# Optimization experiments

Measured on AMD Instinct MI355X. Metric: run time of the kernel, lower is better.

Reference implementation:

```python
import jax, jax.numpy as jnp
import numpy as np

EPS = 1e-12  # F.normalize default eps: clamps norm from below


def _l2_normalize(x):
    n = jnp.sqrt(jnp.sum(x * x, axis=-1, keepdims=True))
    return x / jnp.maximum(n, EPS)


def setup_inputs() -> dict:
    key = jax.random.key(0)
    kq, kk = jax.random.split(key)
    B, N, D = 256, 65536, 3072
    query = jax.random.normal(kq, (B, D), dtype=jnp.float32)
    keys = jax.random.normal(kk, (N, D), dtype=jnp.float32)
    return {"query": query, "keys": keys, "k": 10}


def reference(query, keys, k):
    # torch.nan_to_num(query, nan=0.0, posinf=1.0, neginf=-1.0)
    q = jnp.nan_to_num(query, nan=0.0, posinf=1.0, neginf=-1.0)
    q_norm = _l2_normalize(q)            # (B, D)
    keys_norm = _l2_normalize(keys)      # (N, D) -- precomputed buffer in torch
    scores = jnp.einsum('bd,nd->bn', q_norm, keys_norm)  # cosine sims (B, N)
    _, topk_idx = jax.lax.top_k(scores, k)               # (B, k)
    top_k_embeddings = keys[topk_idx]                    # gather raw embeddings (B, k, D)
    return top_k_embeddings, topk_idx
```

## Files before the change

kernel.cpp:

```cpp
#include <hip/hip_runtime.h>
#include <math.h>

#define NQ 256
#define NK 65536
#define DD 3072
#define TOPK 10
#define BN 64
#define BK 64
#define KTILES (DD / BK)
#define ATILE_BYTES (256 * BK * 2)

typedef unsigned long long u64;
typedef unsigned int u32;
typedef unsigned short u16;

typedef __attribute__((ext_vector_type(8))) short short8;
typedef __attribute__((ext_vector_type(4))) float f32x4;
typedef __attribute__((ext_vector_type(4))) unsigned short us4;

#define GLDS(src, dst)                                                        \
  __builtin_amdgcn_global_load_lds(                                           \
      (const __attribute__((address_space(1))) void*)(src),                   \
      (__attribute__((address_space(3))) void*)(dst), 16, 0, 0)

__device__ __forceinline__ float fixv(float x) {
  if (isnan(x)) return 0.0f;
  if (isinf(x)) return x > 0.0f ? 1.0f : -1.0f;
  return x;
}

__device__ __forceinline__ u16 f2bf(float x) {
  u32 u = __float_as_uint(x);
  u32 r = (u + 0x7fffu + ((u >> 16) & 1u)) >> 16;
  return (u16)r;
}

__device__ __forceinline__ u64 makekey(float f, int idx) {
  u32 u = __float_as_uint(f);
  u = (u & 0x80000000u) ? ~u : (u | 0x80000000u);
  return ((u64)u << 32) | (u32)(~(u32)idx);
}

__global__ __launch_bounds__(256) void qnorm_kernel(const float* __restrict__ query,
                                                    float* __restrict__ qn,
                                                    u16* __restrict__ apre) {
  const int m = blockIdx.x;
  const int t = threadIdx.x;
  const float4* qp = (const float4*)(query + (size_t)m * DD);
  float4 v[3];
  float s = 0.0f;
#pragma unroll
  for (int i = 0; i < 3; ++i) {
    float4 x = qp[t + i * 256];
    x.x = fixv(x.x); x.y = fixv(x.y); x.z = fixv(x.z); x.w = fixv(x.w);
    v[i] = x;
    s += x.x * x.x + x.y * x.y + x.z * x.z + x.w * x.w;
  }
#pragma unroll
  for (int off = 32; off > 0; off >>= 1) s += __shfl_xor(s, off);
  __shared__ float red[4];
  if ((t & 63) == 0) red[t >> 6] = s;
  __syncthreads();
  float inv = 1.0f / fmaxf(sqrtf(red[0] + red[1] + red[2] + red[3]), 1e-12f);
#pragma unroll
  for (int i = 0; i < 3; ++i) {
    float4 x = v[i];
    x.x *= inv; x.y *= inv; x.z *= inv; x.w *= inv;
    ((float4*)(qn + (size_t)m * DD))[t + i * 256] = x;
    int k0 = (t + i * 256) * 4;
    int kt = k0 >> 6;
    int kk = k0 & 63;
    u32 off = (u32)kt * ATILE_BYTES + (((u32)(m * 128 + kk * 2)) ^ (((u32)m & 7) << 4));
    us4 b;
    b.x = f2bf(x.x); b.y = f2bf(x.y); b.z = f2bf(x.z); b.w = f2bf(x.w);
    *(us4*)((char*)apre + off) = b;
  }
}

__global__ __launch_bounds__(256, 3) void gemm_kernel(const u16* __restrict__ apre,
                                                      const float* __restrict__ keys,
                                                      float* __restrict__ invk,
                                                      float* __restrict__ scores) {
  __shared__ __align__(16) u16 As[256 * BK];
  __shared__ __align__(16) u16 Bs[BN * BK];
  __shared__ float sinv[BN];
  const int t = threadIdx.x;
  const int w = t >> 6, l = t & 63;
  const int n0 = blockIdx.x * BN;

  f32x4 acc[4][4];
#pragma unroll
  for (int mi = 0; mi < 4; ++mi)
#pragma unroll
    for (int ni = 0; ni < 4; ++ni) acc[mi][ni] = (f32x4){0.f, 0.f, 0.f, 0.f};
  float ssq[4] = {0.f, 0.f, 0.f, 0.f};

  const int br = t >> 4;
  const int bc = (t & 15) * 4;

  for (int kt = 0; kt < KTILES; ++kt) {
    __syncthreads();
    const char* asrc = (const char*)apre + (size_t)kt * ATILE_BYTES;
#pragma unroll
    for (int i = 0; i < 8; ++i)
      GLDS(asrc + i * 4096 + t * 16, (char*)As + i * 4096 + t * 16);
    const int kb = kt * BK;
#pragma unroll
    for (int i = 0; i < 4; ++i) {
      int row = i * 16 + br;
      float4 v = *(const float4*)(keys + (size_t)(n0 + row) * DD + kb + bc);
      ssq[i] += v.x * v.x + v.y * v.y + v.z * v.z + v.w * v.w;
      us4 b;
      b.x = f2bf(v.x); b.y = f2bf(v.y); b.z = f2bf(v.z); b.w = f2bf(v.w);
      u32 off = ((u32)(row * 128 + bc * 2)) ^ (((u32)row & 7) << 4);
      *(us4*)((char*)Bs + off) = b;
    }
    __syncthreads();
#pragma unroll
    for (int ks = 0; ks < 2; ++ks) {
      short8 a[4], b[4];
#pragma unroll
      for (int mi = 0; mi < 4; ++mi) {
        int row = w * 64 + mi * 16 + (l & 15);
        u32 off = ((u32)(row * 128 + ks * 64 + (l >> 4) * 16)) ^ (((u32)row & 7) << 4);
        a[mi] = *(const short8*)((const char*)As + off);
      }
#pragma unroll
      for (int ni = 0; ni < 4; ++ni) {
        int row = ni * 16 + (l & 15);
        u32 off = ((u32)(row * 128 + ks * 64 + (l >> 4) * 16)) ^ (((u32)row & 7) << 4);
        b[ni] = *(const short8*)((const char*)Bs + off);
      }
#pragma unroll
      for (int mi = 0; mi < 4; ++mi)
#pragma unroll
        for (int ni = 0; ni < 4; ++ni)
          acc[mi][ni] = __builtin_amdgcn_mfma_f32_16x16x32_bf16(a[mi], b[ni], acc[mi][ni], 0, 0, 0);
    }
  }

#pragma unroll
  for (int i = 0; i < 4; ++i) {
    float s = ssq[i];
    s += __shfl_xor(s, 1); s += __shfl_xor(s, 2);
    s += __shfl_xor(s, 4); s += __shfl_xor(s, 8);
    ssq[i] = s;
  }
  if ((t & 15) == 0) {
#pragma unroll
    for (int i = 0; i < 4; ++i) {
      int row = i * 16 + br;
      float iv = 1.0f / fmaxf(sqrtf(ssq[i]), 1e-12f);
      sinv[row] = iv;
      invk[n0 + row] = iv;
    }
  }
  __syncthreads();

#pragma unroll
  for (int ni = 0; ni < 4; ++ni) {
    int nl = ni * 16 + (l & 15);
    float iv = sinv[nl];
#pragma unroll
    for (int mi = 0; mi < 4; ++mi) {
      int q = w * 64 + mi * 16 + (l >> 4) * 4;
#pragma unroll
      for (int r = 0; r < 4; ++r)
        scores[(size_t)(q + r) * NK + n0 + nl] = acc[mi][ni][r] * iv;
    }
  }
}

__global__ __launch_bounds__(256) void topk_part(const float* __restrict__ scores,
                                                 u64* __restrict__ cand) {
  const int b = blockIdx.x >> 3, p = blockIdx.x & 7;
  const int t = threadIdx.x;
  const int w = t >> 6, l = t & 63;
  const float4* row4 = (const float4*)(scores + (size_t)b * NK) + p * 2048;

  float4 v[8];
#pragma unroll
  for (int i = 0; i < 8; ++i) v[i] = row4[i * 256 + t];

  u64 c16[16];
#pragma unroll
  for (int i = 0; i < 4; ++i) {
    int nb = (p * 2048 + i * 256 + t) * 4;
    c16[i * 4 + 0] = makekey(v[i].x, nb + 0);
    c16[i * 4 + 1] = makekey(v[i].y, nb + 1);
    c16[i * 4 + 2] = makekey(v[i].z, nb + 2);
    c16[i * 4 + 3] = makekey(v[i].w, nb + 3);
  }
  u64 mn = c16[0];
#pragma unroll
  for (int i = 1; i < 16; ++i) mn = c16[i] < mn ? c16[i] : mn;

#pragma unroll
  for (int i = 4; i < 8; ++i) {
    int nb = (p * 2048 + i * 256 + t) * 4;
    float e[4] = {v[i].x, v[i].y, v[i].z, v[i].w};
#pragma unroll
    for (int j = 0; j < 4; ++j) {
      u64 kk = makekey(e[j], nb + j);
      if (kk > mn) {
#pragma unroll
        for (int q = 0; q < 16; ++q)
          if (c16[q] == mn) c16[q] = kk;
        u64 m2 = c16[0];
#pragma unroll
        for (int q = 1; q < 16; ++q) m2 = c16[q] < m2 ? c16[q] : m2;
        mn = m2;
      }
    }
  }

#pragma unroll 1
  for (int r = 0; r < 16; ++r) {
    u64 best = 0;
#pragma unroll
    for (int i = 0; i < 16; ++i) best = c16[i] > best ? c16[i] : best;
    u64 wb = best;
#pragma unroll
    for (int off = 1; off < 64; off <<= 1) {
      u64 o = __shfl_xor(wb, off);
      wb = o > wb ? o : wb;
    }
#pragma unroll
    for (int i = 0; i < 16; ++i)
      if (c16[i] == wb) c16[i] = 0;
    if (l == 0) cand[(((size_t)b * 8 + p) * 4 + w) * 16 + r] = wb;
  }
}

__global__ __launch_bounds__(256) void merge_rescore(const u64* __restrict__ cand,
                                                     const float* __restrict__ qn,
                                                     const float* __restrict__ keys,
                                                     const float* __restrict__ invk,
                                                     float* __restrict__ out_emb,
                                                     float* __restrict__ out_idx) {
  const int b = blockIdx.x;
  const int t = threadIdx.x;
  const int w = t >> 6, l = t & 63;
  __shared__ u64 top16[16];
  __shared__ float exact[16];
  __shared__ int ord[TOPK];

  if (w == 0) {
    u64 lc[8];
    const u64* cb = cand + (size_t)b * 512;
#pragma unroll
    for (int i = 0; i < 8; ++i) lc[i] = cb[l * 8 + i];
#pragma unroll 1
    for (int r = 0; r < 16; ++r) {
      u64 best = 0;
#pragma unroll
      for (int i = 0; i < 8; ++i) best = lc[i] > best ? lc[i] : best;
      u64 wb = best;
#pragma unroll
      for (int off = 1; off < 64; off <<= 1) {
        u64 o = __shfl_xor(wb, off);
        wb = o > wb ? o : wb;
      }
#pragma unroll
      for (int i = 0; i < 8; ++i)
        if (lc[i] == wb) lc[i] = 0;
      if (l == 0) top16[r] = wb;
    }
  }
  __syncthreads();

  {
    const int g = t >> 4, c = t & 15;
    const int idx = (int)(~(u32)top16[g]);
    const float iv = invk[idx];
    const float4* kp = (const float4*)(keys + (size_t)idx * DD);
    const float4* qp = (const float4*)(qn + (size_t)b * DD);
    float s = 0.0f;
    for (int j = 0; j < 48; ++j) {
      float4 kv = kp[j * 16 + c];
      float4 qv = qp[j * 16 + c];
      s = fmaf(qv.x, kv.x * iv, s);
      s = fmaf(qv.y, kv.y * iv, s);
      s = fmaf(qv.z, kv.z * iv, s);
      s = fmaf(qv.w, kv.w * iv, s);
    }
    s += __shfl_xor(s, 1); s += __shfl_xor(s, 2);
    s += __shfl_xor(s, 4); s += __shfl_xor(s, 8);
    if (c == 0) exact[g] = s;
  }
  __syncthreads();

  if (w == 0 && l < 16) {
    u64 ek = makekey(exact[l], (int)(~(u32)top16[l]));
#pragma unroll 1
    for (int r = 0; r < TOPK; ++r) {
      u64 wb = ek;
#pragma unroll
      for (int off = 1; off < 16; off <<= 1) {
        u64 o = __shfl_xor(wb, off);
        wb = o > wb ? o : wb;
      }
      if (wb == ek) ek = 0;
      if (l == 0) ord[r] = (int)(~(u32)wb);
    }
  }
  __syncthreads();

  for (int r = 0; r < TOPK; ++r) {
    int idx = ord[r];
    if (t == 0) out_idx[b * TOPK + r] = (float)idx;
    const float4* src = (const float4*)(keys + (size_t)idx * DD);
    float4* dst = (float4*)(out_emb + ((size_t)b * TOPK + r) * DD);
#pragma unroll
    for (int c2 = 0; c2 < 3; ++c2) dst[t + c2 * 256] = src[t + c2 * 256];
  }
}

extern "C" void kernel_launch(void* const* d_in, const int* in_sizes, int n_in,
                              void* d_out, int out_size, void* d_ws, size_t ws_size,
                              hipStream_t stream) {
  const float* query = (const float*)d_in[0];
  const float* keys  = (const float*)d_in[1];

  float* ws = (float*)d_ws;
  float* invk   = ws;
  float* qn     = ws + NK;
  u16*   apre   = (u16*)(ws + NK + (size_t)NQ * DD);
  float* scores = ws + NK + (size_t)NQ * DD + (size_t)KTILES * 256 * BK / 2;
  u64*   cand   = (u64*)(scores + (size_t)NQ * NK);

  float* out_emb = (float*)d_out;
  float* out_idx = (float*)d_out + (size_t)NQ * TOPK * DD;

  qnorm_kernel<<<NQ, 256, 0, stream>>>(query, qn, apre);
  gemm_kernel<<<NK / BN, 256, 0, stream>>>(apre, keys, invk, scores);
  topk_part<<<NQ * 8, 256, 0, stream>>>(scores, cand);
  merge_rescore<<<NQ, 256, 0, stream>>>(cand, qn, keys, invk, out_emb, out_idx);
}
```

Baseline: 323.9 us.

## Fuse per-tile top-k selection into GEMM epilogue and prefetch key tiles

```diff
diff --git a/kernel.cpp b/kernel.cpp
--- a/kernel.cpp
+++ b/kernel.cpp
@@ -9,6 +9,7 @@
 #define BK 64
 #define KTILES (DD / BK)
 #define ATILE_BYTES (256 * BK * 2)
+#define CPB 8
 
 typedef unsigned long long u64;
 typedef unsigned int u32;
@@ -39,6 +40,12 @@
   u32 u = __float_as_uint(f);
   u = (u & 0x80000000u) ? ~u : (u | 0x80000000u);
   return ((u64)u << 32) | (u32)(~(u32)idx);
+}
+
+__device__ __forceinline__ u64 skey(u16 bf, int idx) {
+  u32 s = ((u32)bf) << 16;
+  s = (s & 0x80000000u) ? ~s : (s | 0x80000000u);
+  return ((u64)s << 32) | (u32)(~(u32)idx);
 }
 
 __global__ __launch_bounds__(256) void qnorm_kernel(const float* __restrict__ query,
@@ -77,10 +84,10 @@
   }
 }
 
-__global__ __launch_bounds__(256, 3) void gemm_kernel(const u16* __restrict__ apre,
-                                                      const float* __restrict__ keys,
-                                                      float* __restrict__ invk,
-                                                      float* __restrict__ scores) {
+__global__ __launch_bounds__(256, 3) void gemm_topk(const u16* __restrict__ apre,
+                                                    const float* __restrict__ keys,
+                                                    float* __restrict__ invk,
+                                                    u64* __restrict__ cand) {
   __shared__ __align__(16) u16 As[256 * BK];
   __shared__ __align__(16) u16 Bs[BN * BK];
   __shared__ float sinv[BN];
@@ -98,24 +105,34 @@
   const int br = t >> 4;
   const int bc = (t & 15) * 4;
 
+  float4 bpf[4];
+#pragma unroll
+  for (int i = 0; i < 4; ++i)
+    bpf[i] = *(const float4*)(keys + (size_t)(n0 + i * 16 + br) * DD + bc);
+
   for (int kt = 0; kt < KTILES; ++kt) {
     __syncthreads();
     const char* asrc = (const char*)apre + (size_t)kt * ATILE_BYTES;
 #pragma unroll
     for (int i = 0; i < 8; ++i)
       GLDS(asrc + i * 4096 + t * 16, (char*)As + i * 4096 + t * 16);
-    const int kb = kt * BK;
 #pragma unroll
     for (int i = 0; i < 4; ++i) {
-      int row = i * 16 + br;
-      float4 v = *(const float4*)(keys + (size_t)(n0 + row) * DD + kb + bc);
+      float4 v = bpf[i];
       ssq[i] += v.x * v.x + v.y * v.y + v.z * v.z + v.w * v.w;
       us4 b;
       b.x = f2bf(v.x); b.y = f2bf(v.y); b.z = f2bf(v.z); b.w = f2bf(v.w);
+      int row = i * 16 + br;
       u32 off = ((u32)(row * 128 + bc * 2)) ^ (((u32)row & 7) << 4);
       *(us4*)((char*)Bs + off) = b;
     }
     __syncthreads();
+    if (kt < KTILES - 1) {
+      const int kb = (kt + 1) * BK;
+#pragma unroll
+      for (int i = 0; i < 4; ++i)
+        bpf[i] = *(const float4*)(keys + (size_t)(n0 + i * 16 + br) * DD + kb + bc);
+    }
 #pragma unroll
     for (int ks = 0; ks < 2; ++ks) {
       short8 a[4], b[4];
@@ -163,73 +180,47 @@
     float iv = sinv[nl];
 #pragma unroll
     for (int mi = 0; mi < 4; ++mi) {
-      int q = w * 64 + mi * 16 + (l >> 4) * 4;
-#pragma unroll
-      for (int r = 0; r < 4; ++r)
-        scores[(size_t)(q + r) * NK + n0 + nl] = acc[mi][ni][r] * iv;
-    }
-  }
-}
-
-__global__ __launch_bounds__(256) void topk_part(const float* __restrict__ scores,
-                                                 u64* __restrict__ cand) {
-  const int b = blockIdx.x >> 3, p = blockIdx.x & 7;
-  const int t = threadIdx.x;
-  const int w = t >> 6, l = t & 63;
-  const float4* row4 = (const float4*)(scores + (size_t)b * NK) + p * 2048;
-
-  float4 v[8];
-#pragma unroll
-  for (int i = 0; i < 8; ++i) v[i] = row4[i * 256 + t];
-
-  u64 c16[16];
-#pragma unroll
-  for (int i = 0; i < 4; ++i) {
-    int nb = (p * 2048 + i * 256 + t) * 4;
-    c16[i * 4 + 0] = makekey(v[i].x, nb + 0);
-    c16[i * 4 + 1] = makekey(v[i].y, nb + 1);
-    c16[i * 4 + 2] = makekey(v[i].z, nb + 2);
-    c16[i * 4 + 3] = makekey(v[i].w, nb + 3);
-  }
-  u64 mn = c16[0];
-#pragma unroll
-  for (int i = 1; i < 16; ++i) mn = c16[i] < mn ? c16[i] : mn;
-
-#pragma unroll
-  for (int i = 4; i < 8; ++i) {
-    int nb = (p * 2048 + i * 256 + t) * 4;
-    float e[4] = {v[i].x, v[i].y, v[i].z, v[i].w};
-#pragma unroll
-    for (int j = 0; j < 4; ++j) {
-      u64 kk = makekey(e[j], nb + j);
+      int qb = w * 64 + mi * 16 + (l >> 4) * 4;
+#pragma unroll
+      for (int r = 0; r < 4; ++r) {
+        int q = qb + r;
+        u16 bf = f2bf(acc[mi][ni][r] * iv);
+        u32 off = ((u32)(q * 128 + nl * 2)) ^ (((u32)q & 7) << 4);
+        *(u16*)((char*)As + off) = bf;
+      }
+    }
+  }
+  __syncthreads();
+
+  u64 c8[CPB];
+  {
+    short8 v = *(const short8*)((const char*)As + (((u32)(t * 128)) ^ (((u32)t & 7) << 4)));
+#pragma unroll
+    for (int j = 0; j < 8; ++j) c8[j] = skey((u16)v[j], n0 + j);
+  }
+  u64 mn = c8[0];
+#pragma unroll
+  for (int i = 1; i < CPB; ++i) mn = c8[i] < mn ? c8[i] : mn;
+#pragma unroll
+  for (int c = 1; c < 8; ++c) {
+    short8 v = *(const short8*)((const char*)As + (((u32)(t * 128 + c * 16)) ^ (((u32)t & 7) << 4)));
+#pragma unroll
+    for (int j = 0; j < 8; ++j) {
+      u64 kk = skey((u16)v[j], n0 + c * 8 + j);
       if (kk > mn) {
 #pragma unroll
-        for (int q = 0; q < 16; ++q)
-          if (c16[q] == mn) c16[q] = kk;
-        u64 m2 = c16[0];
-#pragma unroll
-        for (int q = 1; q < 16; ++q) m2 = c16[q] < m2 ? c16[q] : m2;
+        for (int q = 0; q < CPB; ++q)
+          if (c8[q] == mn) c8[q] = kk;
+        u64 m2 = c8[0];
+#pragma unroll
+        for (int q = 1; q < CPB; ++q) m2 = c8[q] < m2 ? c8[q] : m2;
         mn = m2;
       }
     }
   }
-
-#pragma unroll 1
-  for (int r = 0; r < 16; ++r) {
-    u64 best = 0;
-#pragma unroll
-    for (int i = 0; i < 16; ++i) best = c16[i] > best ? c16[i] : best;
-    u64 wb = best;
-#pragma unroll
-    for (int off = 1; off < 64; off <<= 1) {
-      u64 o = __shfl_xor(wb, off);
-      wb = o > wb ? o : wb;
-    }
-#pragma unroll
-    for (int i = 0; i < 16; ++i)
-      if (c16[i] == wb) c16[i] = 0;
-    if (l == 0) cand[(((size_t)b * 8 + p) * 4 + w) * 16 + r] = wb;
-  }
+  u64* cp = cand + ((size_t)t * (NK / BN) + blockIdx.x) * CPB;
+#pragma unroll
+  for (int i = 0; i < CPB; ++i) cp[i] = c8[i];
 }
 
 __global__ __launch_bounds__(256) void merge_rescore(const u64* __restrict__ cand,
@@ -241,29 +232,59 @@
   const int b = blockIdx.x;
   const int t = threadIdx.x;
   const int w = t >> 6, l = t & 63;
+  __shared__ u64 wtop[64];
   __shared__ u64 top16[16];
   __shared__ float exact[16];
   __shared__ int ord[TOPK];
 
+  const u64* cb = cand + (size_t)b * (NK / BN) * CPB;
+  u64 c16[16];
+#pragma unroll
+  for (int i = 0; i < 16; ++i) c16[i] = cb[t * 32 + i];
+  u64 mn = c16[0];
+#pragma unroll
+  for (int i = 1; i < 16; ++i) mn = c16[i] < mn ? c16[i] : mn;
+#pragma unroll
+  for (int i = 16; i < 32; ++i) {
+    u64 kk = cb[t * 32 + i];
+    if (kk > mn) {
+#pragma unroll
+      for (int q = 0; q < 16; ++q)
+        if (c16[q] == mn) c16[q] = kk;
+      u64 m2 = c16[0];
+#pragma unroll
+      for (int q = 1; q < 16; ++q) m2 = c16[q] < m2 ? c16[q] : m2;
+      mn = m2;
+    }
+  }
+#pragma unroll 1
+  for (int r = 0; r < 16; ++r) {
+    u64 best = 0;
+#pragma unroll
+    for (int i = 0; i < 16; ++i) best = c16[i] > best ? c16[i] : best;
+    u64 wb = best;
+#pragma unroll
+    for (int off = 1; off < 64; off <<= 1) {
+      u64 o = __shfl_xor(wb, off);
+      wb = o > wb ? o : wb;
+    }
+#pragma unroll
+    for (int i = 0; i < 16; ++i)
+      if (c16[i] == wb) c16[i] = 0;
+    if (l == 0) wtop[w * 16 + r] = wb;
+  }
+  __syncthreads();
   if (w == 0) {
-    u64 lc[8];
-    const u64* cb = cand + (size_t)b * 512;
-#pragma unroll
-    for (int i = 0; i < 8; ++i) lc[i] = cb[l * 8 + i];
+    u64 e = wtop[l];
 #pragma unroll 1
     for (int r = 0; r < 16; ++r) {
-      u64 best = 0;
-#pragma unroll
-      for (int i = 0; i < 8; ++i) best = lc[i] > best ? lc[i] : best;
-      u64 wb = best;
+      u64 wb = e;
 #pragma unroll
       for (int off = 1; off < 64; off <<= 1) {
         u64 o = __shfl_xor(wb, off);
         wb = o > wb ? o : wb;
       }
-#pragma unroll
-      for (int i = 0; i < 8; ++i)
-        if (lc[i] == wb) lc[i] = 0;
+      if (e == wb) e = 0;
       if (l == 0) top16[r] = wb;
     }
   }
@@ -323,17 +344,15 @@
   const float* keys  = (const float*)d_in[1];
 
   float* ws = (float*)d_ws;
-  float* invk   = ws;
-  float* qn     = ws + NK;
-  u16*   apre   = (u16*)(ws + NK + (size_t)NQ * DD);
-  float* scores = ws + NK + (size_t)NQ * DD + (size_t)KTILES * 256 * BK / 2;
-  u64*   cand   = (u64*)(scores + (size_t)NQ * NK);
+  float* invk = ws;
+  float* qn   = ws + NK;
+  u16*   apre = (u16*)(ws + NK + (size_t)NQ * DD);
+  u64*   cand = (u64*)((char*)(void*)apre + (size_t)KTILES * ATILE_BYTES);
 
   float* out_emb = (float*)d_out;
   float* out_idx = (float*)d_out + (size_t)NQ * TOPK * DD;
 
   qnorm_kernel<<<NQ, 256, 0, stream>>>(query, qn, apre);
-  gemm_kernel<<<NK / BN, 256, 0, stream>>>(apre, keys, invk, scores);
-  topk_part<<<NQ * 8, 256, 0, stream>>>(scores, cand);
+  gemm_topk<<<NK / BN, 256, 0, stream>>>(apre, keys, invk, cand);
   merge_rescore<<<NQ, 256, 0, stream>>>(cand, qn, keys, invk, out_emb, out_idx);
 }
```

Result: slower. 332.6 us (+2.7%).

## Double-buffer fp32 key tiles via direct LDS loads and read A fragments from global

Applied to the files above, without the earlier changes.

```diff
diff --git a/kernel.cpp b/kernel.cpp
--- a/kernel.cpp
+++ b/kernel.cpp
@@ -8,7 +8,6 @@
 #define BN 64
 #define BK 64
 #define KTILES (DD / BK)
-#define ATILE_BYTES (256 * BK * 2)
 
 typedef unsigned long long u64;
 typedef unsigned int u32;
@@ -17,6 +16,7 @@
 typedef __attribute__((ext_vector_type(8))) short short8;
 typedef __attribute__((ext_vector_type(4))) float f32x4;
 typedef __attribute__((ext_vector_type(4))) unsigned short us4;
+typedef __attribute__((ext_vector_type(4))) unsigned int u32x4;
 
 #define GLDS(src, dst)                                                        \
   __builtin_amdgcn_global_load_lds(                                           \
@@ -70,10 +70,9 @@
     int k0 = (t + i * 256) * 4;
     int kt = k0 >> 6;
     int kk = k0 & 63;
-    u32 off = (u32)kt * ATILE_BYTES + (((u32)(m * 128 + kk * 2)) ^ (((u32)m & 7) << 4));
     us4 b;
     b.x = f2bf(x.x); b.y = f2bf(x.y); b.z = f2bf(x.z); b.w = f2bf(x.w);
-    *(us4*)((char*)apre + off) = b;
+    *(us4*)(apre + ((size_t)kt * 256 + m) * 64 + kk) = b;
   }
 }
 
@@ -81,8 +80,7 @@
                                                       const float* __restrict__ keys,
                                                       float* __restrict__ invk,
                                                       float* __restrict__ scores) {
-  __shared__ __align__(16) u16 As[256 * BK];
-  __shared__ __align__(16) u16 Bs[BN * BK];
+  __shared__ __align__(16) float Bf[2][BN * BK];
   __shared__ float sinv[BN];
   const int t = threadIdx.x;
   const int w = t >> 6, l = t & 63;
@@ -93,64 +91,86 @@
   for (int mi = 0; mi < 4; ++mi)
 #pragma unroll
     for (int ni = 0; ni < 4; ++ni) acc[mi][ni] = (f32x4){0.f, 0.f, 0.f, 0.f};
-  float ssq[4] = {0.f, 0.f, 0.f, 0.f};
-
-  const int br = t >> 4;
-  const int bc = (t & 15) * 4;
+  float ssq_acc = 0.0f;
+
+#define STAGE_B(kt_, buf_)                                                    \
+  {                                                                           \
+    const int kb_ = (kt_)*BK;                                                 \
+    _Pragma("unroll")                                                         \
+    for (int i_ = 0; i_ < 4; ++i_) {                                          \
+      int c_ = w * 256 + i_ * 64 + l;                                         \
+      int row_ = c_ >> 4;                                                     \
+      int kc_ = (c_ & 15) ^ (row_ & 7);                                       \
+      GLDS(keys + (size_t)(n0 + row_) * DD + kb_ + kc_ * 4,                   \
+           (char*)&Bf[buf_][0] + c_ * 16);                                    \
+    }                                                                         \
+  }
+
+  STAGE_B(0, 0);
 
   for (int kt = 0; kt < KTILES; ++kt) {
     __syncthreads();
-    const char* asrc = (const char*)apre + (size_t)kt * ATILE_BYTES;
-#pragma unroll
-    for (int i = 0; i < 8; ++i)
-      GLDS(asrc + i * 4096 + t * 16, (char*)As + i * 4096 + t * 16);
-    const int kb = kt * BK;
-#pragma unroll
-    for (int i = 0; i < 4; ++i) {
-      int row = i * 16 + br;
-      float4 v = *(const float4*)(keys + (size_t)(n0 + row) * DD + kb + bc);
-      ssq[i] += v.x * v.x + v.y * v.y + v.z * v.z + v.w * v.w;
-      us4 b;
-      b.x = f2bf(v.x); b.y = f2bf(v.y); b.z = f2bf(v.z); b.w = f2bf(v.w);
-      u32 off = ((u32)(row * 128 + bc * 2)) ^ (((u32)row & 7) << 4);
-      *(us4*)((char*)Bs + off) = b;
-    }
-    __syncthreads();
+    const int cur = kt & 1;
+
+    short8 af[8];
+    {
+      const u16* ab = apre + (size_t)kt * 256 * 64;
+#pragma unroll
+      for (int mi = 0; mi < 4; ++mi)
+#pragma unroll
+        for (int ks = 0; ks < 2; ++ks)
+          af[mi * 2 + ks] = *(const short8*)(ab +
+              (size_t)(w * 64 + mi * 16 + (l & 15)) * 64 + ks * 32 + (l >> 4) * 8);
+    }
+    __builtin_amdgcn_sched_barrier(0);
+    if (kt + 1 < KTILES) STAGE_B(kt + 1, cur ^ 1);
+    __builtin_amdgcn_sched_barrier(0);
+
+    {
+      const int row = t >> 2;
+#pragma unroll
+      for (int j = 0; j < 4; ++j) {
+        int kc = (t & 3) * 4 + j;
+        f32x4 v = *(const f32x4*)((const char*)&Bf[cur][0] +
+                                  (row * 16 + (kc ^ (row & 7))) * 16);
+        ssq_acc += v.x * v.x + v.y * v.y + v.z * v.z + v.w * v.w;
+      }
+    }
+
 #pragma unroll
     for (int ks = 0; ks < 2; ++ks) {
-      short8 a[4], b[4];
-#pragma unroll
-      for (int mi = 0; mi < 4; ++mi) {
-        int row = w * 64 + mi * 16 + (l & 15);
-        u32 off = ((u32)(row * 128 + ks * 64 + (l >> 4) * 16)) ^ (((u32)row & 7) << 4);
-        a[mi] = *(const short8*)((const char*)As + off);
-      }
+      short8 b[4];
 #pragma unroll
       for (int ni = 0; ni < 4; ++ni) {
         int row = ni * 16 + (l & 15);
-        u32 off = ((u32)(row * 128 + ks * 64 + (l >> 4) * 16)) ^ (((u32)row & 7) << 4);
-        b[ni] = *(const short8*)((const char*)Bs + off);
+        int kc0 = ks * 8 + (l >> 4) * 2;
+        u32x4 p0 = *(const u32x4*)((const char*)&Bf[cur][0] +
+                                   (row * 16 + (kc0 ^ (row & 7))) * 16);
+        u32x4 p1 = *(const u32x4*)((const char*)&Bf[cur][0] +
+                                   (row * 16 + ((kc0 + 1) ^ (row & 7))) * 16);
+        u32x4 bw;
+        bw.x = (p0.x >> 16) | (p0.y & 0xffff0000u);
+        bw.y = (p0.z >> 16) | (p0.w & 0xffff0000u);
+        bw.z = (p1.x >> 16) | (p1.y & 0xffff0000u);
+        bw.w = (p1.z >> 16) | (p1.w & 0xffff0000u);
+        b[ni] = *(short8*)&bw;
       }
 #pragma unroll
       for (int mi = 0; mi < 4; ++mi)
 #pragma unroll
         for (int ni = 0; ni < 4; ++ni)
-          acc[mi][ni] = __builtin_amdgcn_mfma_f32_16x16x32_bf16(a[mi], b[ni], acc[mi][ni], 0, 0, 0);
-    }
-  }
-
-#pragma unroll
-  for (int i = 0; i < 4; ++i) {
-    float s = ssq[i];
-    s += __shfl_xor(s, 1); s += __shfl_xor(s, 2);
-    s += __shfl_xor(s, 4); s += __shfl_xor(s, 8);
-    ssq[i] = s;
-  }
-  if ((t & 15) == 0) {
-#pragma unroll
-    for (int i = 0; i < 4; ++i) {
-      int row = i * 16 + br;
-      float iv = 1.0f / fmaxf(sqrtf(ssq[i]), 1e-12f);
+          acc[mi][ni] = __builtin_amdgcn_mfma_f32_16x16x32_bf16(
+              af[mi * 2 + ks], b[ni], acc[mi][ni], 0, 0, 0);
+    }
+  }
+
+  {
+    float s = ssq_acc;
+    s += __shfl_xor(s, 1);
+    s += __shfl_xor(s, 2);
+    if ((t & 3) == 0) {
+      int row = t >> 2;
+      float iv = 1.0f / fmaxf(sqrtf(s), 1e-12f);
       sinv[row] = iv;
       invk[n0 + row] = iv;
     }
```

Result: slower. 390.7 us (+20.6%).

## Widen GEMM blocks to 512 threads, fuse top-k with merge, split gather

Applied to the files above, without the earlier changes.

```diff
diff --git a/kernel.cpp b/kernel.cpp
--- a/kernel.cpp
+++ b/kernel.cpp
@@ -77,7 +77,7 @@
   }
 }
 
-__global__ __launch_bounds__(256, 3) void gemm_kernel(const u16* __restrict__ apre,
+__global__ __launch_bounds__(512, 4) void gemm_kernel(const u16* __restrict__ apre,
                                                       const float* __restrict__ keys,
                                                       float* __restrict__ invk,
                                                       float* __restrict__ scores) {
@@ -88,40 +88,43 @@
   const int w = t >> 6, l = t & 63;
   const int n0 = blockIdx.x * BN;
 
-  f32x4 acc[4][4];
-#pragma unroll
-  for (int mi = 0; mi < 4; ++mi)
+  f32x4 acc[2][4];
+#pragma unroll
+  for (int mi = 0; mi < 2; ++mi)
 #pragma unroll
     for (int ni = 0; ni < 4; ++ni) acc[mi][ni] = (f32x4){0.f, 0.f, 0.f, 0.f};
-  float ssq[4] = {0.f, 0.f, 0.f, 0.f};
-
-  const int br = t >> 4;
-  const int bc = (t & 15) * 4;
+  float ssq = 0.0f;
+
+  const int brow = t >> 3;
+  const int bco = (t & 7) * 8;
 
   for (int kt = 0; kt < KTILES; ++kt) {
     __syncthreads();
     const char* asrc = (const char*)apre + (size_t)kt * ATILE_BYTES;
 #pragma unroll
-    for (int i = 0; i < 8; ++i)
-      GLDS(asrc + i * 4096 + t * 16, (char*)As + i * 4096 + t * 16);
+    for (int i = 0; i < 4; ++i)
+      GLDS(asrc + i * 8192 + t * 16, (char*)As + i * 8192 + t * 16);
     const int kb = kt * BK;
-#pragma unroll
-    for (int i = 0; i < 4; ++i) {
-      int row = i * 16 + br;
-      float4 v = *(const float4*)(keys + (size_t)(n0 + row) * DD + kb + bc);
-      ssq[i] += v.x * v.x + v.y * v.y + v.z * v.z + v.w * v.w;
-      us4 b;
-      b.x = f2bf(v.x); b.y = f2bf(v.y); b.z = f2bf(v.z); b.w = f2bf(v.w);
-      u32 off = ((u32)(row * 128 + bc * 2)) ^ (((u32)row & 7) << 4);
-      *(us4*)((char*)Bs + off) = b;
+    {
+      const float* bp = keys + (size_t)(n0 + brow) * DD + kb + bco;
+      float4 v0 = *(const float4*)(bp);
+      float4 v1 = *(const float4*)(bp + 4);
+      ssq += v0.x * v0.x + v0.y * v0.y + v0.z * v0.z + v0.w * v0.w +
+             v1.x * v1.x + v1.y * v1.y + v1.z * v1.z + v1.w * v1.w;
+      us4 b0, b1;
+      b0.x = f2bf(v0.x); b0.y = f2bf(v0.y); b0.z = f2bf(v0.z); b0.w = f2bf(v0.w);
+      b1.x = f2bf(v1.x); b1.y = f2bf(v1.y); b1.z = f2bf(v1.z); b1.w = f2bf(v1.w);
+      u32 off = ((u32)(brow * 128 + bco * 2)) ^ (((u32)brow & 7) << 4);
+      *(us4*)((char*)Bs + off) = b0;
+      *(us4*)((char*)Bs + off + 8) = b1;
     }
     __syncthreads();
 #pragma unroll
     for (int ks = 0; ks < 2; ++ks) {
-      short8 a[4], b[4];
-#pragma unroll
-      for (int mi = 0; mi < 4; ++mi) {
-        int row = w * 64 + mi * 16 + (l & 15);
+      short8 a[2], b[4];
+#pragma unroll
+      for (int mi = 0; mi < 2; ++mi) {
+        int row = w * 32 + mi * 16 + (l & 15);
         u32 off = ((u32)(row * 128 + ks * 64 + (l >> 4) * 16)) ^ (((u32)row & 7) << 4);
         a[mi] = *(const short8*)((const char*)As + off);
       }
@@ -132,27 +135,20 @@
         b[ni] = *(const short8*)((const char*)Bs + off);
       }
 #pragma unroll
-      for (int mi = 0; mi < 4; ++mi)
+      for (int mi = 0; mi < 2; ++mi)
 #pragma unroll
         for (int ni = 0; ni < 4; ++ni)
           acc[mi][ni] = __builtin_amdgcn_mfma_f32_16x16x32_bf16(a[mi], b[ni], acc[mi][ni], 0, 0, 0);
     }
   }
 
-#pragma unroll
-  for (int i = 0; i < 4; ++i) {
-    float s = ssq[i];
-    s += __shfl_xor(s, 1); s += __shfl_xor(s, 2);
-    s += __shfl_xor(s, 4); s += __shfl_xor(s, 8);
-    ssq[i] = s;
-  }
-  if ((t & 15) == 0) {
-#pragma unroll
-    for (int i = 0; i < 4; ++i) {
-      int row = i * 16 + br;
-      float iv = 1.0f / fmaxf(sqrtf(ssq[i]), 1e-12f);
-      sinv[row] = iv;
-      invk[n0 + row] = iv;
+  {
+    float s = ssq;
+    s += __shfl_xor(s, 1); s += __shfl_xor(s, 2); s += __shfl_xor(s, 4);
+    if ((t & 7) == 0) {
+      float iv = 1.0f / fmaxf(sqrtf(s), 1e-12f);
+      sinv[brow] = iv;
+      invk[n0 + brow] = iv;
     }
   }
   __syncthreads();
@@ -162,8 +158,8 @@
     int nl = ni * 16 + (l & 15);
     float iv = sinv[nl];
 #pragma unroll
-    for (int mi = 0; mi < 4; ++mi) {
-      int q = w * 64 + mi * 16 + (l >> 4) * 4;
+    for (int mi = 0; mi < 2; ++mi) {
+      int q = w * 32 + mi * 16 + (l >> 4) * 4;
 #pragma unroll
       for (int r = 0; r < 4; ++r)
         scores[(size_t)(q + r) * NK + n0 + nl] = acc[mi][ni][r] * iv;
@@ -171,34 +167,39 @@
   }
 }
 
-__global__ __launch_bounds__(256) void topk_part(const float* __restrict__ scores,
-                                                 u64* __restrict__ cand) {
-  const int b = blockIdx.x >> 3, p = blockIdx.x & 7;
+__global__ __launch_bounds__(256) void topk_merge(const float* __restrict__ scores,
+                                                  const float* __restrict__ qn,
+                                                  const float* __restrict__ keys,
+                                                  const float* __restrict__ invk,
+                                                  int* __restrict__ ordws,
+                                                  float* __restrict__ out_idx) {
+  const int b = blockIdx.x;
   const int t = threadIdx.x;
   const int w = t >> 6, l = t & 63;
-  const float4* row4 = (const float4*)(scores + (size_t)b * NK) + p * 2048;
-
-  float4 v[8];
-#pragma unroll
-  for (int i = 0; i < 8; ++i) v[i] = row4[i * 256 + t];
+  const float4* row4 = (const float4*)(scores + (size_t)b * NK);
+  __shared__ u64 wtop[64];
+  __shared__ u64 top16[16];
+  __shared__ float exact[16];
 
   u64 c16[16];
 #pragma unroll
   for (int i = 0; i < 4; ++i) {
-    int nb = (p * 2048 + i * 256 + t) * 4;
-    c16[i * 4 + 0] = makekey(v[i].x, nb + 0);
-    c16[i * 4 + 1] = makekey(v[i].y, nb + 1);
-    c16[i * 4 + 2] = makekey(v[i].z, nb + 2);
-    c16[i * 4 + 3] = makekey(v[i].w, nb + 3);
+    float4 v = row4[i * 256 + t];
+    int nb = (i * 256 + t) * 4;
+    c16[i * 4 + 0] = makekey(v.x, nb + 0);
+    c16[i * 4 + 1] = makekey(v.y, nb + 1);
+    c16[i * 4 + 2] = makekey(v.z, nb + 2);
+    c16[i * 4 + 3] = makekey(v.w, nb + 3);
   }
   u64 mn = c16[0];
 #pragma unroll
   for (int i = 1; i < 16; ++i) mn = c16[i] < mn ? c16[i] : mn;
 
-#pragma unroll
-  for (int i = 4; i < 8; ++i) {
-    int nb = (p * 2048 + i * 256 + t) * 4;
-    float e[4] = {v[i].x, v[i].y, v[i].z, v[i].w};
+#pragma unroll 4
+  for (int i = 4; i < 64; ++i) {
+    float4 v = row4[i * 256 + t];
+    int nb = (i * 256 + t) * 4;
+    float e[4] = {v.x, v.y, v.z, v.w};
 #pragma unroll
     for (int j = 0; j < 4; ++j) {
       u64 kk = makekey(e[j], nb + j);
@@ -228,42 +229,20 @@
 #pragma unroll
     for (int i = 0; i < 16; ++i)
       if (c16[i] == wb) c16[i] = 0;
-    if (l == 0) cand[(((size_t)b * 8 + p) * 4 + w) * 16 + r] = wb;
-  }
-}
-
-__global__ __launch_bounds__(256) void merge_rescore(const u64* __restrict__ cand,
-                                                     const float* __restrict__ qn,
-                                                     const float* __restrict__ keys,
-                                                     const float* __restrict__ invk,
-                                                     float* __restrict__ out_emb,
-                                                     float* __restrict__ out_idx) {
-  const int b = blockIdx.x;
-  const int t = threadIdx.x;
-  const int w = t >> 6, l = t & 63;
-  __shared__ u64 top16[16];
-  __shared__ float exact[16];
-  __shared__ int ord[TOPK];
-
+    if (l == 0) wtop[w * 16 + r] = wb;
+  }
+  __syncthreads();
   if (w == 0) {
-    u64 lc[8];
-    const u64* cb = cand + (size_t)b * 512;
-#pragma unroll
-    for (int i = 0; i < 8; ++i) lc[i] = cb[l * 8 + i];
+    u64 e = wtop[l];
 #pragma unroll 1
     for (int r = 0; r < 16; ++r) {
-      u64 best = 0;
-#pragma unroll
-      for (int i = 0; i < 8; ++i) best = lc[i] > best ? lc[i] : best;
-      u64 wb = best;
+      u64 wb = e;
 #pragma unroll
       for (int off = 1; off < 64; off <<= 1) {
         u64 o = __shfl_xor(wb, off);
         wb = o > wb ? o : wb;
       }
-#pragma unroll
-      for (int i = 0; i < 8; ++i)
-        if (lc[i] == wb) lc[i] = 0;
+      if (e == wb) e = 0;
       if (l == 0) top16[r] = wb;
     }
   }
@@ -301,19 +280,24 @@
         wb = o > wb ? o : wb;
       }
       if (wb == ek) ek = 0;
-      if (l == 0) ord[r] = (int)(~(u32)wb);
-    }
-  }
-  __syncthreads();
-
-  for (int r = 0; r < TOPK; ++r) {
-    int idx = ord[r];
-    if (t == 0) out_idx[b * TOPK + r] = (float)idx;
-    const float4* src = (const float4*)(keys + (size_t)idx * DD);
-    float4* dst = (float4*)(out_emb + ((size_t)b * TOPK + r) * DD);
-#pragma unroll
-    for (int c2 = 0; c2 < 3; ++c2) dst[t + c2 * 256] = src[t + c2 * 256];
-  }
+      if (l == 0) {
+        int idx = (int)(~(u32)wb);
+        ordws[b * TOPK + r] = idx;
+        out_idx[b * TOPK + r] = (float)idx;
+      }
+    }
+  }
+}
+
+__global__ __launch_bounds__(256) void gather_kernel(const int* __restrict__ ordws,
+                                                     const float* __restrict__ keys,
+                                                     float* __restrict__ out_emb) {
+  const int t = threadIdx.x;
+  const int idx = ordws[blockIdx.x];
+  const float4* src = (const float4*)(keys + (size_t)idx * DD);
+  float4* dst = (float4*)(out_emb + (size_t)blockIdx.x * DD);
+#pragma unroll
+  for (int c = 0; c < 3; ++c) dst[t + c * 256] = src[t + c * 256];
 }
 
 extern "C" void kernel_launch(void* const* d_in, const int* in_sizes, int n_in,
@@ -327,13 +311,13 @@
   float* qn     = ws + NK;
   u16*   apre   = (u16*)(ws + NK + (size_t)NQ * DD);
   float* scores = ws + NK + (size_t)NQ * DD + (size_t)KTILES * 256 * BK / 2;
-  u64*   cand   = (u64*)(scores + (size_t)NQ * NK);
+  int*   ordws  = (int*)(scores + (size_t)NQ * NK);
 
   float* out_emb = (float*)d_out;
   float* out_idx = (float*)d_out + (size_t)NQ * TOPK * DD;
 
   qnorm_kernel<<<NQ, 256, 0, stream>>>(query, qn, apre);
-  gemm_kernel<<<NK / BN, 256, 0, stream>>>(apre, keys, invk, scores);
-  topk_part<<<NQ * 8, 256, 0, stream>>>(scores, cand);
-  merge_rescore<<<NQ, 256, 0, stream>>>(cand, qn, keys, invk, out_emb, out_idx);
-}
+  gemm_kernel<<<NK / BN, 512, 0, stream>>>(apre, keys, invk, scores);
+  topk_merge<<<NQ, 256, 0, stream>>>(scores, qn, keys, invk, ordws, out_idx);
+  gather_kernel<<<NQ * TOPK, 256, 0, stream>>>(ordws, keys, out_emb);
+}
```

Result: slower. 439.0 us (+35.5%).
